# Performance work log

Hardware: AMD Instinct MI355X
Metric: run time of the kernel (lower is better)

Reference implementation:

```python
import jax, jax.numpy as jnp
import numpy as np

D_MODEL = 1024
D_STATE = 16
D_CONV = 4
EXPAND = 2
D_INNER = EXPAND * D_MODEL          # 2048
DT_RANK = (D_MODEL + 15) // 16      # 64 (mamba 'auto')
B, L = 2, 1024


def _mamba_params(key, scale=0.02):
    ks = jax.random.split(key, 6)
    return dict(
        inW=jax.random.normal(ks[0], (2 * D_INNER, D_MODEL), jnp.float32) * scale,
        convW=jax.random.normal(ks[1], (D_INNER, 1, D_CONV), jnp.float32) * scale,
        convb=jnp.zeros((D_INNER,), jnp.float32),
        xprojW=jax.random.normal(ks[2], (DT_RANK + 2 * D_STATE, D_INNER), jnp.float32) * scale,
        dtW=jax.random.normal(ks[3], (D_INNER, DT_RANK), jnp.float32) * scale,
        dtb=jax.random.normal(ks[4], (D_INNER,), jnp.float32) * scale,
        A_log=jnp.log(jnp.tile(jnp.arange(1, D_STATE + 1, dtype=jnp.float32), (D_INNER, 1))),
        Dskip=jnp.ones((D_INNER,), jnp.float32),
        outW=jax.random.normal(ks[5], (D_MODEL, D_INNER), jnp.float32) * scale,
    )


def setup_inputs() -> dict:
    key = jax.random.key(0)
    kx, kf, kb, kp = jax.random.split(key, 4)
    inp = {"x": jax.random.normal(kx, (B, L, D_MODEL), jnp.float32)}
    inp["ln_w"] = jnp.ones((D_MODEL,), jnp.float32)
    inp["ln_b"] = jnp.zeros((D_MODEL,), jnp.float32)
    for pref, k in (("f_", kf), ("b_", kb)):
        for name, v in _mamba_params(k).items():
            inp[pref + name] = v
    inp["proj_W"] = jax.random.normal(kp, (D_MODEL, 2 * D_MODEL), jnp.float32) * 0.02
    inp["proj_b"] = jnp.zeros((D_MODEL,), jnp.float32)
    return inp


def _layernorm(x, w, b, eps=1e-5):
    mu = jnp.mean(x, axis=-1, keepdims=True)
    var = jnp.var(x, axis=-1, keepdims=True)
    return (x - mu) * jax.lax.rsqrt(var + eps) * w + b


def _mamba(x, inW, convW, convb, xprojW, dtW, dtb, A_log, Dskip, outW):
    # x: [B, L, d_model]
    xz = jnp.einsum('bld,ed->ble', x, inW)           # [B,L,2*d_inner]
    xs, z = jnp.split(xz, 2, axis=-1)                # each [B,L,d_inner]
    # depthwise causal conv over L
    xc = jnp.transpose(xs, (0, 2, 1))                # [B,d_inner,L]
    xc = jax.lax.conv_general_dilated(
        xc, convW, window_strides=(1,), padding=[(D_CONV - 1, 0)],
        feature_group_count=D_INNER)
    xs = jax.nn.silu(jnp.transpose(xc + convb[None, :, None], (0, 2, 1)))
    # input-dependent dt, B, C
    xdb = jnp.einsum('bld,ed->ble', xs, xprojW)      # [B,L,dt_rank+2*d_state]
    dt, Bm, Cm = jnp.split(xdb, [DT_RANK, DT_RANK + D_STATE], axis=-1)
    dt = jax.nn.softplus(jnp.einsum('blr,dr->bld', dt, dtW) + dtb)  # [B,L,d_inner]
    A = -jnp.exp(A_log)                              # [d_inner,d_state], negative
    dA = jnp.exp(dt[..., None] * A)                  # [B,L,d_inner,d_state]
    dBx = dt[..., None] * Bm[:, :, None, :] * xs[..., None]

    def step(h, inputs):
        dA_t, dBx_t, C_t = inputs                    # [B,d,s],[B,d,s],[B,s]
        h = h * dA_t + dBx_t
        y = jnp.einsum('bds,bs->bd', h, C_t)
        return h, y

    h0 = jnp.zeros((x.shape[0], D_INNER, D_STATE), x.dtype)
    _, ys = jax.lax.scan(step, h0, (jnp.moveaxis(dA, 1, 0),
                                    jnp.moveaxis(dBx, 1, 0),
                                    jnp.moveaxis(Cm, 1, 0)))
    y = jnp.moveaxis(ys, 0, 1)                       # [B,L,d_inner]
    y = (y + xs * Dskip) * jax.nn.silu(z)
    return jnp.einsum('bld,ed->ble', y, outW)        # [B,L,d_model]


def reference(x, ln_w, ln_b,
              f_inW, f_convW, f_convb, f_xprojW, f_dtW, f_dtb, f_A_log, f_Dskip, f_outW,
              b_inW, b_convW, b_convb, b_xprojW, b_dtW, b_dtb, b_A_log, b_Dskip, b_outW,
              proj_W, proj_b):
    normed = _layernorm(x, ln_w, ln_b)
    fwd_out = _mamba(normed, f_inW, f_convW, f_convb, f_xprojW, f_dtW, f_dtb,
                     f_A_log, f_Dskip, f_outW)
    bwd_out = _mamba(normed[:, ::-1, :], b_inW, b_convW, b_convb, b_xprojW, b_dtW,
                     b_dtb, b_A_log, b_Dskip, b_outW)[:, ::-1, :]
    combined = jnp.concatenate([fwd_out, bwd_out], axis=-1)
    return x + jnp.einsum('blc,ec->ble', combined, proj_W) + proj_b
```

## Files before the change

### kernel.cpp

```cpp
#include <hip/hip_runtime.h>
#include <hip/hip_bf16.h>
#include <math.h>

#define DM   1024
#define DI   2048
#define DTR  64
#define DST  16
#define NB   2
#define LL   1024
#define MR   (NB*LL)
#define XLD  128
#define KS   8

typedef __bf16 bf16x8 __attribute__((ext_vector_type(8)));
typedef float  f32x4  __attribute__((ext_vector_type(4)));
typedef unsigned short u16x8 __attribute__((ext_vector_type(8)));

__device__ __forceinline__ float siluf(float x) { return x / (1.f + __expf(-x)); }
__device__ __forceinline__ float softplusf(float x) {
    return fmaxf(x, 0.f) + log1pf(__expf(-fabsf(x)));
}
__device__ __forceinline__ unsigned short f2bf(float f) {
    __hip_bfloat16 h = __float2bfloat16(f);
    return *reinterpret_cast<unsigned short*>(&h);
}
__device__ __forceinline__ float bf2f(__hip_bfloat16 h) { return __bfloat162float(h); }
__device__ __forceinline__ float bfu2f(unsigned short u) {
    __hip_bfloat16 h = *reinterpret_cast<__hip_bfloat16*>(&u);
    return __bfloat162float(h);
}

__device__ __forceinline__ void gl2lds16(const __hip_bfloat16* g, __hip_bfloat16* l)
{
    __builtin_amdgcn_global_load_lds(
        (const __attribute__((address_space(1))) unsigned int*)g,
        (__attribute__((address_space(3))) unsigned int*)l, 16, 0, 0);
}

__global__ __launch_bounds__(256) void prep_k(
    const float* __restrict__ s0, const float* __restrict__ s1,
    const float* __restrict__ s2, const float* __restrict__ s3,
    const float* __restrict__ s4, __hip_bfloat16* __restrict__ warena,
    const float* __restrict__ fx, const float* __restrict__ bx,
    __hip_bfloat16* __restrict__ wpb2,
    const float* __restrict__ fo, const float* __restrict__ bo,
    __hip_bfloat16* __restrict__ wot,
    const float* __restrict__ x, const float* __restrict__ lnw,
    const float* __restrict__ lnb, __hip_bfloat16* __restrict__ nb)
{
    __shared__ float pshm[64 * 65];
    const int b = blockIdx.x;
    const int tid = threadIdx.x;

    if (b < 10496) {
        long idx = (long)b * 1024 + tid * 4;
        const float* src; long off;
        if      (idx <  4194304L) { src = s0; off = idx; }
        else if (idx <  8388608L) { src = s1; off = idx -  4194304L; }
        else if (idx < 10485760L) { src = s2; off = idx -  8388608L; }
        else if (idx < 10616832L) { src = s3; off = idx - 10485760L; }
        else                      { src = s4; off = idx - 10616832L; }
        float4 v = *(const float4*)(src + off);
        ushort4 o;
        o.x = f2bf(v.x); o.y = f2bf(v.y); o.z = f2bf(v.z); o.w = f2bf(v.w);
        *(ushort4*)((unsigned short*)warena + idx) = o;
    } else if (b < 10624) {
        int t = b - 10496;
        int z = t >> 6;
        const float* in = z ? bx : fx;
        int idx = ((t & 63) * 256 + tid) * 4;
        int row = idx >> 11;
        ushort4 o = make_ushort4(0, 0, 0, 0);
        if (row < 96) {
            float4 v = *(const float4*)(in + idx);
            o.x = f2bf(v.x); o.y = f2bf(v.y); o.z = f2bf(v.z); o.w = f2bf(v.w);
        }
        *(ushort4*)((unsigned short*)wpb2 + (size_t)z * 128 * DI + idx) = o;
    } else if (b < 11648) {
        int t = b - 10624;
        int z = t >> 9; t &= 511;
        const float* src = z ? bo : fo;
        int c0 = (t & 31) * 64;
        int r0 = (t >> 5) * 64;
        int tc = tid & 63;
        int tr = tid >> 6;
        #pragma unroll
        for (int ii = 0; ii < 16; ++ii) {
            int rl = tr + ii * 4;
            pshm[tc * 65 + rl] = src[(size_t)(r0 + rl) * DI + c0 + tc];
        }
        __syncthreads();
        __hip_bfloat16* dst = wot + (size_t)z * DI * DM;
        #pragma unroll
        for (int ii = 0; ii < 16; ++ii) {
            int cl = tr + ii * 4;
            dst[(size_t)(c0 + cl) * DM + r0 + tc] = __float2bfloat16(pshm[cl * 65 + tc]);
        }
    } else {
        int row = b - 11648;
        const float* xr = x + (size_t)row * DM;
        float4 v = *(const float4*)(xr + tid * 4);
        float s = v.x + v.y + v.z + v.w;
        float q = v.x*v.x + v.y*v.y + v.z*v.z + v.w*v.w;
        #pragma unroll
        for (int off = 32; off > 0; off >>= 1) {
            s += __shfl_xor(s, off, 64);
            q += __shfl_xor(q, off, 64);
        }
        int wv = tid >> 6;
        if ((tid & 63) == 0) { pshm[wv] = s; pshm[8 + wv] = q; }
        __syncthreads();
        s = pshm[0] + pshm[1] + pshm[2] + pshm[3];
        q = pshm[8] + pshm[9] + pshm[10] + pshm[11];
        float mu  = s * (1.f / DM);
        float var = q * (1.f / DM) - mu * mu;
        float rstd = rsqrtf(var + 1e-5f);
        float4 wv4 = *(const float4*)(lnw + tid * 4);
        float4 bv4 = *(const float4*)(lnb + tid * 4);
        ushort4 o;
        o.x = f2bf((v.x - mu) * rstd * wv4.x + bv4.x);
        o.y = f2bf((v.y - mu) * rstd * wv4.y + bv4.y);
        o.z = f2bf((v.z - mu) * rstd * wv4.z + bv4.z);
        o.w = f2bf((v.w - mu) * rstd * wv4.w + bv4.w);
        *(ushort4*)((unsigned short*)nb + (size_t)row * DM + tid * 4) = o;
    }
}

__global__ __launch_bounds__(512) void inproj256_k(
    const __hip_bfloat16* __restrict__ A,
    const __hip_bfloat16* __restrict__ Bmat,
    __hip_bfloat16* __restrict__ C)
{
    __shared__ __hip_bfloat16 smem[65536];
    const int tid = threadIdx.x;
    int id = blockIdx.x;
    int s  = (id & 7) * 32 + (id >> 3);
    const int z  = s >> 7;
    const int r  = s & 127;
    const int bm = (r & 7) * 256;
    const int bn = (r >> 3) * 256;
    const __hip_bfloat16* Az = A;
    const __hip_bfloat16* Bz = Bmat + (size_t)z * 2 * DI * DM;
    __hip_bfloat16* Cz = C + (size_t)z * MR * 2 * DI;

    const int wv   = tid >> 6;
    const int lane = tid & 63;
    const int wm   = wv >> 2;
    const int wn   = wv & 3;
    const int fr   = lane & 15;
    const int quad = lane >> 4;

    const int srow = tid >> 2;
    const int scol = 8 * ((tid & 3) ^ ((tid >> 3) & 3));
    const int kph  = (quad ^ ((fr >> 1) & 3)) * 8;

    __hip_bfloat16* const Asl = smem;
    __hip_bfloat16* const Bsl = smem + 32768;

    f32x4 acc[8][4] = {};
    bf16x8 aF[4], bB[4];

#define STG_A(TAU, KK) { \
    const int ub_ = (((TAU) & 1) * 2 + (KK)) * 8192; \
    const int gc_ = (TAU) * 64 + (KK) * 32 + scol; \
    gl2lds16(Az + (size_t)(bm + srow) * DM + gc_,       Asl + ub_ + tid * 8); \
    gl2lds16(Az + (size_t)(bm + 128 + srow) * DM + gc_, Asl + ub_ + 4096 + tid * 8); }
#define STG_B(TAU, KK) { \
    const int ub_ = (((TAU) & 1) * 2 + (KK)) * 8192; \
    const int gc_ = (TAU) * 64 + (KK) * 32 + scol; \
    gl2lds16(Bz + (size_t)(bn + srow) * DM + gc_,       Bsl + ub_ + tid * 8); \
    gl2lds16(Bz + (size_t)(bn + 128 + srow) * DM + gc_, Bsl + ub_ + 4096 + tid * 8); }

#define RD_A(BUF, KK, MH) { \
    const __hip_bfloat16* p_ = Asl + ((BUF) * 2 + (KK)) * 8192 + kph; \
    _Pragma("unroll") for (int i = 0; i < 4; ++i) \
        aF[i] = *(const bf16x8*)(p_ + (wm * 128 + (MH) * 64 + i * 16 + fr) * 32); }
#define RD_B(BUF, KK) { \
    const __hip_bfloat16* p_ = Bsl + ((BUF) * 2 + (KK)) * 8192 + kph; \
    _Pragma("unroll") for (int j = 0; j < 4; ++j) \
        bB[j] = *(const bf16x8*)(p_ + (wn * 64 + j * 16 + fr) * 32); }

#define PHASE(BUF, KK, MH, STGC, T1, T2, VMC) { \
    if ((MH) == 0) { RD_B(BUF, KK); } \
    RD_A(BUF, KK, MH); \
    if ((STGC) == 1) { STG_A((T1), 1); } \
    if ((STGC) == 2) { STG_B((T1), 1); } \
    if ((STGC) == 3) { STG_A((T2), 0); } \
    if ((STGC) == 4) { STG_B((T2), 0); } \
    asm volatile("s_barrier" ::: "memory"); \
    asm volatile("s_waitcnt lgkmcnt(0)" ::: "memory"); \
    __builtin_amdgcn_sched_barrier(0); \
    __builtin_amdgcn_s_setprio(1); \
    _Pragma("unroll") for (int i = 0; i < 4; ++i) \
        _Pragma("unroll") for (int j = 0; j < 4; ++j) \
            acc[(MH) * 4 + i][j] = __builtin_amdgcn_mfma_f32_16x16x32_bf16( \
                aF[i], bB[j], acc[(MH) * 4 + i][j], 0, 0, 0); \
    __builtin_amdgcn_s_setprio(0); \
    if ((VMC) == 8) { asm volatile("s_waitcnt vmcnt(8)" ::: "memory"); } \
    if ((VMC) == 4) { asm volatile("s_waitcnt vmcnt(4)" ::: "memory"); } \
    if ((VMC) == 1) { asm volatile("s_waitcnt vmcnt(0)" ::: "memory"); } \
    asm volatile("s_barrier" ::: "memory"); }

    STG_A(0, 0); STG_B(0, 0); STG_A(0, 1); STG_B(0, 1); STG_A(1, 0); STG_B(1, 0);
    asm volatile("s_waitcnt vmcnt(8)" ::: "memory");
    asm volatile("s_barrier" ::: "memory");

    #pragma unroll 1
    for (int t = 0; t < 14; ++t) {
        const int buf = t & 1;
        const int t1 = t + 1, t2 = t + 2;
        PHASE(buf, 0, 0, 1, t1, t2, 0);
        PHASE(buf, 0, 1, 2, t1, t2, 8);
        PHASE(buf, 1, 0, 3, t1, t2, 0);
        PHASE(buf, 1, 1, 4, t1, t2, 8);
    }
    PHASE(0, 0, 0, 1, 15, 0, 0);
    PHASE(0, 0, 1, 2, 15, 0, 8);
    PHASE(0, 1, 0, 0, 0, 0, 0);
    PHASE(0, 1, 1, 0, 0, 0, 4);
    PHASE(1, 0, 0, 0, 0, 0, 0);
    PHASE(1, 0, 1, 0, 0, 0, 1);
    PHASE(1, 1, 0, 0, 0, 0, 0);
    PHASE(1, 1, 1, 0, 0, 0, 0);

#undef PHASE
#undef RD_A
#undef RD_B
#undef STG_A
#undef STG_B

    float* eps = (float*)smem;
    const int orow = tid >> 3;
    const int ocol = (tid & 7) * 32;
    #pragma unroll
    for (int p = 0; p < 4; ++p) {
        __syncthreads();
        if (wm == (p >> 1)) {
            int ib = (p & 1) * 4;
            #pragma unroll
            for (int i2 = 0; i2 < 4; ++i2)
                #pragma unroll
                for (int j = 0; j < 4; ++j)
                    #pragma unroll
                    for (int rr = 0; rr < 4; ++rr)
                        eps[(i2 * 16 + quad * 4 + rr) * 260 + wn * 64 + j * 16 + fr]
                            = acc[ib + i2][j][rr];
        }
        __syncthreads();
        unsigned short os[32] __attribute__((aligned(16)));
        #pragma unroll
        for (int c = 0; c < 32; ++c) os[c] = f2bf(eps[orow * 260 + ocol + c]);
        unsigned short* dst = (unsigned short*)Cz +
            (size_t)(bm + p * 64 + orow) * (2 * DI) + bn + ocol;
        *(uint4*)(dst +  0) = *(const uint4*)(os +  0);
        *(uint4*)(dst +  8) = *(const uint4*)(os +  8);
        *(uint4*)(dst + 16) = *(const uint4*)(os + 16);
        *(uint4*)(dst + 24) = *(const uint4*)(os + 24);
    }
}

template<int EPI>
__global__ __launch_bounds__(256) void gemm_gl(
    const __hip_bfloat16* __restrict__ A, int lda, size_t aofs,
    const __hip_bfloat16* __restrict__ B, int ldb, size_t bofs,
    void* __restrict__ Cp, int ldc, size_t cofs, int K,
    const float* __restrict__ bias0, const float* __restrict__ bias1)
{
    __shared__ __hip_bfloat16 smem[2 * 128 * 64];
    __hip_bfloat16* As = smem;
    __hip_bfloat16* Bs = smem + 128 * 64;
    const int tid  = threadIdx.x;
    const int z    = blockIdx.z;
    const int bm   = blockIdx.y * 128;
    const int bn   = blockIdx.x * 128;
    const __hip_bfloat16* Az = A + (size_t)z * aofs;
    const __hip_bfloat16* Bz = B + (size_t)z * bofs;
    const int wv   = tid >> 6;
    const int lane = tid & 63;
    const int wr   = (wv >> 1) * 64;
    const int wc   = (wv & 1) * 64;
    const int srow = wv * 32 + (lane >> 3);
    const int cg   = ((lane & 7) ^ (lane >> 3)) * 8;
    const int fr   = lane & 15;
    const int quad = lane >> 4;
    const int pc0  = (quad ^ (fr & 7)) * 8;
    const int pc1  = ((4 + quad) ^ (fr & 7)) * 8;

    f32x4 acc[4][4] = {};

    for (int k0 = 0; k0 < K; k0 += 64) {
        __syncthreads();
        #pragma unroll
        for (int i = 0; i < 4; ++i) {
            int r = srow + i * 8;
            gl2lds16(Az + (size_t)(bm + r) * lda + k0 + cg, As + wv * 2048 + i * 512);
            gl2lds16(Bz + (size_t)(bn + r) * ldb + k0 + cg, Bs + wv * 2048 + i * 512);
        }
        __syncthreads();
        #pragma unroll
        for (int kk = 0; kk < 2; ++kk) {
            const int pc = kk ? pc1 : pc0;
            bf16x8 af[4], bf_[4];
            #pragma unroll
            for (int i = 0; i < 4; ++i) {
                af[i]  = *(const bf16x8*)(As + (wr + i * 16 + fr) * 64 + pc);
                bf_[i] = *(const bf16x8*)(Bs + (wc + i * 16 + fr) * 64 + pc);
            }
            #pragma unroll
            for (int i = 0; i < 4; ++i)
                #pragma unroll
                for (int j = 0; j < 4; ++j)
                    acc[i][j] = __builtin_amdgcn_mfma_f32_16x16x32_bf16(
                        af[i], bf_[j], acc[i][j], 0, 0, 0);
        }
    }

    const float* bias = (EPI == 3) ? (z ? bias1 : bias0) : nullptr;
    float* eps = (float*)smem;
    const int half = wv >> 1;
    const int lrow = tid >> 3;
    const int cseg = (tid & 7) * 16;
    const int gr_  = bm + (lrow >> 4) * 64 + (lrow & 15);
    #pragma unroll
    for (int i = 0; i < 4; ++i) {
        __syncthreads();
        #pragma unroll
        for (int j = 0; j < 4; ++j)
            #pragma unroll
            for (int r = 0; r < 4; ++r)
                eps[(half * 16 + quad * 4 + r) * 132 + wc + j * 16 + fr] = acc[i][j][r];
        __syncthreads();
        float vals[16];
        *(float4*)(vals +  0) = *(const float4*)(eps + lrow * 132 + cseg +  0);
        *(float4*)(vals +  4) = *(const float4*)(eps + lrow * 132 + cseg +  4);
        *(float4*)(vals +  8) = *(const float4*)(eps + lrow * 132 + cseg +  8);
        *(float4*)(vals + 12) = *(const float4*)(eps + lrow * 132 + cseg + 12);
        int gr = gr_ + i * 16;
        int gc = bn + cseg;
        if (EPI == 0) {
            float* dst = (float*)Cp + (size_t)z * cofs + (size_t)gr * ldc + gc;
            *(float4*)(dst +  0) = *(const float4*)(vals +  0);
            *(float4*)(dst +  4) = *(const float4*)(vals +  4);
            *(float4*)(dst +  8) = *(const float4*)(vals +  8);
            *(float4*)(dst + 12) = *(const float4*)(vals + 12);
        } else {
            unsigned short os[16];
            #pragma unroll
            for (int c = 0; c < 16; ++c) {
                float t = vals[c];
                if (EPI == 3) t = softplusf(t + bias[gc + c]);
                os[c] = f2bf(t);
            }
            unsigned short* dst = (unsigned short*)Cp + (size_t)z * cofs +
                                  (size_t)gr * ldc + gc;
            *(ushort4*)(dst +  0) = *(ushort4*)(os +  0);
            *(ushort4*)(dst +  4) = *(ushort4*)(os +  4);
            *(ushort4*)(dst +  8) = *(ushort4*)(os +  8);
            *(ushort4*)(dst + 12) = *(ushort4*)(os + 12);
        }
    }
}

__global__ __launch_bounds__(256) void xproj_part_k(
    const __hip_bfloat16* __restrict__ A,
    const __hip_bfloat16* __restrict__ B,
    float* __restrict__ part)
{
    __shared__ __hip_bfloat16 smem[2 * 128 * 64];
    __hip_bfloat16* As = smem;
    __hip_bfloat16* Bs = smem + 128 * 64;
    const int tid  = threadIdx.x;
    const int ks   = blockIdx.x;
    const int bm   = blockIdx.y * 128;
    const int z    = blockIdx.z;
    const __hip_bfloat16* Az = A + (size_t)z * MR * DI;
    const __hip_bfloat16* Bz = B + (size_t)z * 128 * DI;
    const int kb   = ks * (DI / KS);
    const int wv   = tid >> 6;
    const int lane = tid & 63;
    const int wr   = (wv >> 1) * 64;
    const int wc   = (wv & 1) * 64;
    const int srow = wv * 32 + (lane >> 3);
    const int cg   = ((lane & 7) ^ (lane >> 3)) * 8;
    const int fr   = lane & 15;
    const int quad = lane >> 4;
    const int pc0  = (quad ^ (fr & 7)) * 8;
    const int pc1  = ((4 + quad) ^ (fr & 7)) * 8;

    f32x4 acc[4][4] = {};

    #pragma unroll
    for (int k0 = 0; k0 < DI / KS; k0 += 64) {
        __syncthreads();
        #pragma unroll
        for (int i = 0; i < 4; ++i) {
            int r = srow + i * 8;
            gl2lds16(Az + (size_t)(bm + r) * DI + kb + k0 + cg, As + wv * 2048 + i * 512);
            gl2lds16(Bz + (size_t)r * DI + kb + k0 + cg,        Bs + wv * 2048 + i * 512);
        }
        __syncthreads();
        #pragma unroll
        for (int kk = 0; kk < 2; ++kk) {
            const int pc = kk ? pc1 : pc0;
            bf16x8 af[4], bf_[4];
            #pragma unroll
            for (int i = 0; i < 4; ++i) {
                af[i]  = *(const bf16x8*)(As + (wr + i * 16 + fr) * 64 + pc);
                bf_[i] = *(const bf16x8*)(Bs + (wc + i * 16 + fr) * 64 + pc);
            }
            #pragma unroll
            for (int i = 0; i < 4; ++i)
                #pragma unroll
                for (int j = 0; j < 4; ++j)
                    acc[i][j] = __builtin_amdgcn_mfma_f32_16x16x32_bf16(
                        af[i], bf_[j], acc[i][j], 0, 0, 0);
        }
    }

    float* dst = part + ((size_t)z * KS + ks) * MR * XLD;
    const int er = quad * 4;
    #pragma unroll
    for (int i = 0; i < 4; ++i)
        #pragma unroll
        for (int j = 0; j < 4; ++j) {
            int row = bm + wr + i * 16 + er;
            int col = wc + j * 16 + fr;
            #pragma unroll
            for (int r = 0; r < 4; ++r)
                dst[(size_t)(row + r) * XLD + col] = acc[i][j][r];
        }
}

__global__ __launch_bounds__(256) void xproj_reduce_k(
    const float* __restrict__ part, float* __restrict__ xdb,
    __hip_bfloat16* __restrict__ xdbt)
{
    int z = blockIdx.y;
    size_t idx = ((size_t)blockIdx.x * 256 + threadIdx.x) * 4;
    const float* p = part + (size_t)z * KS * MR * XLD;
    float4 s = make_float4(0.f, 0.f, 0.f, 0.f);
    #pragma unroll
    for (int ks = 0; ks < KS; ++ks) {
        float4 v = *(const float4*)(p + (size_t)ks * MR * XLD + idx);
        s.x += v.x; s.y += v.y; s.z += v.z; s.w += v.w;
    }
    *(float4*)(xdb + (size_t)z * MR * XLD + idx) = s;
    int c = (int)(idx & (XLD - 1));
    if (c < 64) {
        size_t m = idx >> 7;
        ushort4 o;
        o.x = f2bf(s.x); o.y = f2bf(s.y); o.z = f2bf(s.z); o.w = f2bf(s.w);
        *(ushort4*)((unsigned short*)xdbt + (size_t)z * MR * 64 + m * 64 + c) = o;
    }
}

__global__ __launch_bounds__(256) void conv_silu_k(
    const __hip_bfloat16* __restrict__ xz2,
    const float* __restrict__ fW, const float* __restrict__ fb,
    const float* __restrict__ bW, const float* __restrict__ bb_,
    __hip_bfloat16* __restrict__ xsb2)
{
    const int dirv  = blockIdx.y;
    const int chunk = blockIdx.x;
    const int bb    = chunk >> 8;
    const int t0    = (chunk & 255) * 4;
    const int d     = threadIdx.x * 8;

    const float* w    = (dirv ? bW : fW) + d * 4;
    const float* bias = (dirv ? bb_ : fb) + d;
    const unsigned short* xz =
        (const unsigned short*)(xz2 + (size_t)dirv * MR * 2 * DI) + d;

    u16x8 rows[7];
    #pragma unroll
    for (int rr = 0; rr < 7; ++rr) {
        int t = dirv ? (t0 + rr) : (t0 - 3 + rr);
        bool ok = dirv ? (t < LL) : (t >= 0);
        u16x8 v = {};
        if (ok) v = *(const u16x8*)(xz + (size_t)(bb * LL + t) * (2 * DI));
        rows[rr] = v;
    }
    float wq[8][4];
    #pragma unroll
    for (int c = 0; c < 8; ++c) {
        float4 t = *(const float4*)(w + c * 4);
        if (dirv) { wq[c][0] = t.w; wq[c][1] = t.z; wq[c][2] = t.y; wq[c][3] = t.x; }
        else      { wq[c][0] = t.x; wq[c][1] = t.y; wq[c][2] = t.z; wq[c][3] = t.w; }
    }
    float4 b0 = *(const float4*)(bias);
    float4 b1 = *(const float4*)(bias + 4);
    float bs[8] = {b0.x, b0.y, b0.z, b0.w, b1.x, b1.y, b1.z, b1.w};

    unsigned short* outp = (unsigned short*)xsb2 + (size_t)dirv * MR * DI +
                           (size_t)(bb * LL + t0) * DI + d;
    #pragma unroll
    for (int o = 0; o < 4; ++o) {
        unsigned short os[8] __attribute__((aligned(16)));
        #pragma unroll
        for (int c = 0; c < 8; ++c) {
            float a = bs[c];
            #pragma unroll
            for (int k = 0; k < 4; ++k)
                a = fmaf(wq[c][k], bfu2f(rows[o + k][c]), a);
            os[c] = f2bf(siluf(a));
        }
        *(uint4*)(outp + (size_t)o * DI) = *(const uint4*)os;
    }
}

__global__ __launch_bounds__(256) void scan1_k(
    const __hip_bfloat16* __restrict__ dtf2, const __hip_bfloat16* __restrict__ xsb2,
    const float* __restrict__ xdb2,
    const float* __restrict__ fA, const float* __restrict__ bA,
    float* __restrict__ hend, float* __restrict__ aprod, int G, int Cn)
{
    int d  = blockIdx.x * 256 + threadIdx.x;
    int bb = blockIdx.y;
    int zz = blockIdx.z;
    int dirv = (zz >= G) ? 1 : 0;
    int g = zz - (dirv ? G : 0);
    const float* A_log = dirv ? bA : fA;
    const __hip_bfloat16* dtf = dtf2 + (size_t)dirv * MR * DI;
    const __hip_bfloat16* xs = xsb2 + (size_t)dirv * MR * DI;
    const float* xdb = xdb2 + (size_t)dirv * MR * XLD;
    size_t hoff = (size_t)dirv * G * (NB * DI * DST);

    float Ad[DST], h[DST], ap[DST];
    bool pw = true;
    #pragma unroll
    for (int s = 0; s < DST; ++s) {
        Ad[s] = -__expf(A_log[d * DST + s]);
        pw = pw && (fabsf(Ad[s] + (float)(s + 1)) < 1e-3f * (s + 1));
        h[s] = 0.f; ap[s] = 1.f;
    }
    int i0 = g * Cn;
    for (int i = 0; i < Cn; ++i) {
        int ii = i0 + i;
        int t = dirv ? (LL - 1 - ii) : ii;
        size_t m = (size_t)bb * LL + t;
        float dtv = bf2f(dtf[m * DI + d]);
        float xv  = bf2f(xs[m * DI + d]);
        const float* bc = xdb + m * XLD;
        float dtx = dtv * xv;
        float dAv[DST];
        if (pw) {
            float r = __expf(-dtv);
            float a = r;
            #pragma unroll
            for (int s = 0; s < DST; ++s) { dAv[s] = a; a *= r; }
        } else {
            #pragma unroll
            for (int s = 0; s < DST; ++s) dAv[s] = __expf(dtv * Ad[s]);
        }
        #pragma unroll
        for (int s = 0; s < DST; ++s) {
            h[s] = fmaf(h[s], dAv[s], dtx * bc[64 + s]);
            ap[s] *= dAv[s];
        }
    }
    size_t base = hoff + ((size_t)(g * NB + bb) * DI + d) * DST;
    #pragma unroll
    for (int s = 0; s < DST; s += 4) {
        *(float4*)(hend  + base + s) = make_float4(h[s], h[s+1], h[s+2], h[s+3]);
        *(float4*)(aprod + base + s) = make_float4(ap[s], ap[s+1], ap[s+2], ap[s+3]);
    }
}

__global__ __launch_bounds__(256) void scan2_k(
    float* __restrict__ hend, const float* __restrict__ aprod, int G)
{
    int dirv = blockIdx.y;
    int idx = blockIdx.x * 256 + threadIdx.x;
    const int slab = NB * DI * DST;
    size_t hoff = (size_t)dirv * G * slab;
    float carry = 0.f;
    for (int g = 0; g < G; ++g) {
        size_t off = hoff + (size_t)g * slab + idx;
        float a = aprod[off];
        float e = hend[off];
        hend[off] = carry;
        carry = fmaf(a, carry, e);
    }
}

__global__ __launch_bounds__(256) void scan3_k(
    const __hip_bfloat16* __restrict__ dtf2, const __hip_bfloat16* __restrict__ xsb2,
    const float* __restrict__ xdb2, const __hip_bfloat16* __restrict__ xz2,
    const float* __restrict__ fA, const float* __restrict__ bA,
    const float* __restrict__ fD, const float* __restrict__ bD,
    const float* __restrict__ hin, __hip_bfloat16* __restrict__ ycat, int G, int Cn)
{
    int d  = blockIdx.x * 256 + threadIdx.x;
    int bb = blockIdx.y;
    int zz = blockIdx.z;
    int dirv = (zz >= G) ? 1 : 0;
    int g = zz - (dirv ? G : 0);
    const float* A_log = dirv ? bA : fA;
    const float* Dskip = dirv ? bD : fD;
    const __hip_bfloat16* dtf = dtf2 + (size_t)dirv * MR * DI;
    const __hip_bfloat16* xs = xsb2 + (size_t)dirv * MR * DI;
    const float* xdb = xdb2 + (size_t)dirv * MR * XLD;
    const __hip_bfloat16* xz = xz2 + (size_t)dirv * MR * 2 * DI;
    size_t hoff = (size_t)dirv * G * (NB * DI * DST);

    float Ad[DST], h[DST];
    bool pw = true;
    size_t base = hoff + ((size_t)(g * NB + bb) * DI + d) * DST;
    #pragma unroll
    for (int s = 0; s < DST; ++s) {
        Ad[s] = -__expf(A_log[d * DST + s]);
        pw = pw && (fabsf(Ad[s] + (float)(s + 1)) < 1e-3f * (s + 1));
        h[s] = hin[base + s];
    }
    float Dsk = Dskip[d];
    int i0 = g * Cn;
    for (int i = 0; i < Cn; ++i) {
        int ii = i0 + i;
        int t = dirv ? (LL - 1 - ii) : ii;
        size_t m = (size_t)bb * LL + t;
        float dtv = bf2f(dtf[m * DI + d]);
        float xv  = bf2f(xs[m * DI + d]);
        const float* bc = xdb + m * XLD;
        float dtx = dtv * xv;
        float dAv[DST];
        if (pw) {
            float r = __expf(-dtv);
            float a = r;
            #pragma unroll
            for (int s = 0; s < DST; ++s) { dAv[s] = a; a *= r; }
        } else {
            #pragma unroll
            for (int s = 0; s < DST; ++s) dAv[s] = __expf(dtv * Ad[s]);
        }
        float yv = 0.f;
        #pragma unroll
        for (int s = 0; s < DST; ++s) {
            h[s] = fmaf(h[s], dAv[s], dtx * bc[64 + s]);
            yv = fmaf(h[s], bc[80 + s], yv);
        }
        float zv = bf2f(xz[m * (2 * DI) + DI + d]);
        ycat[m * (2 * DI) + (size_t)dirv * DI + d] =
            __float2bfloat16((yv + xv * Dsk) * siluf(zv));
    }
}

__global__ __launch_bounds__(256) void scan_mono_k(
    const __hip_bfloat16* __restrict__ dtf2, const __hip_bfloat16* __restrict__ xsb2,
    const float* __restrict__ xdb2, const __hip_bfloat16* __restrict__ xz2,
    const float* __restrict__ fA, const float* __restrict__ bA,
    const float* __restrict__ fD, const float* __restrict__ bD,
    __hip_bfloat16* __restrict__ ycat)
{
    int d  = blockIdx.x * 256 + threadIdx.x;
    int bb = blockIdx.y;
    int dirv = blockIdx.z;
    const float* A_log = dirv ? bA : fA;
    const float* Dskip = dirv ? bD : fD;
    const __hip_bfloat16* dtf = dtf2 + (size_t)dirv * MR * DI;
    const __hip_bfloat16* xs = xsb2 + (size_t)dirv * MR * DI;
    const float* xdb = xdb2 + (size_t)dirv * MR * XLD;
    const __hip_bfloat16* xz = xz2 + (size_t)dirv * MR * 2 * DI;
    float Ad[DST], h[DST];
    #pragma unroll
    for (int s = 0; s < DST; ++s) { Ad[s] = -__expf(A_log[d * DST + s]); h[s] = 0.f; }
    float Dsk = Dskip[d];
    for (int i = 0; i < LL; ++i) {
        int t = dirv ? (LL - 1 - i) : i;
        size_t m = (size_t)bb * LL + t;
        float dtv = bf2f(dtf[m * DI + d]);
        float xv  = bf2f(xs[m * DI + d]);
        const float* bc = xdb + m * XLD;
        float dtx = dtv * xv;
        float yv = 0.f;
        #pragma unroll
        for (int s = 0; s < DST; ++s) {
            float dA = __expf(dtv * Ad[s]);
            h[s] = fmaf(h[s], dA, dtx * bc[64 + s]);
            yv = fmaf(h[s], bc[80 + s], yv);
        }
        float zv = bf2f(xz[m * (2 * DI) + DI + d]);
        ycat[m * (2 * DI) + (size_t)dirv * DI + d] =
            __float2bfloat16((yv + xv * Dsk) * siluf(zv));
    }
}

__global__ __launch_bounds__(256) void final_reduce_k(
    const float* __restrict__ part, const float* __restrict__ x,
    const float* __restrict__ proj_b, float* __restrict__ out)
{
    size_t idx = ((size_t)blockIdx.x * 256 + threadIdx.x) * 4;
    float4 s = make_float4(0.f, 0.f, 0.f, 0.f);
    #pragma unroll
    for (int z = 0; z < 4; ++z) {
        float4 v = *(const float4*)(part + (size_t)z * MR * DM + idx);
        s.x += v.x; s.y += v.y; s.z += v.z; s.w += v.w;
    }
    float4 xv = *(const float4*)(x + idx);
    float4 pb = *(const float4*)(proj_b + (idx & (DM - 1)));
    float4 o;
    o.x = xv.x + pb.x + s.x;
    o.y = xv.y + pb.y + s.y;
    o.z = xv.z + pb.z + s.z;
    o.w = xv.w + pb.w + s.w;
    *(float4*)(out + idx) = o;
}

extern "C" void kernel_launch(void* const* d_in, const int* in_sizes, int n_in,
                              void* d_out, int out_size, void* d_ws, size_t ws_size,
                              hipStream_t stream)
{
    const float* x      = (const float*)d_in[0];
    const float* ln_w   = (const float*)d_in[1];
    const float* ln_b   = (const float*)d_in[2];
    const float* f_inW    = (const float*)d_in[3];
    const float* f_convW  = (const float*)d_in[4];
    const float* f_convb  = (const float*)d_in[5];
    const float* f_xprojW = (const float*)d_in[6];
    const float* f_dtW    = (const float*)d_in[7];
    const float* f_dtb    = (const float*)d_in[8];
    const float* f_A_log  = (const float*)d_in[9];
    const float* f_Dskip  = (const float*)d_in[10];
    const float* f_outW   = (const float*)d_in[11];
    const float* b_inW    = (const float*)d_in[12];
    const float* b_convW  = (const float*)d_in[13];
    const float* b_convb  = (const float*)d_in[14];
    const float* b_xprojW = (const float*)d_in[15];
    const float* b_dtW    = (const float*)d_in[16];
    const float* b_dtb    = (const float*)d_in[17];
    const float* b_A_log  = (const float*)d_in[18];
    const float* b_Dskip  = (const float*)d_in[19];
    const float* b_outW   = (const float*)d_in[20];
    const float* proj_W = (const float*)d_in[21];
    const float* proj_b = (const float*)d_in[22];

    float* ws = (float*)d_ws;
    size_t o = 0;
    __hip_bfloat16* xz2  = (__hip_bfloat16*)(ws + o);
    float* fpart = ws + o;
    o += (size_t)2 * MR * 2 * DI / 2;
    __hip_bfloat16* xsb2 = (__hip_bfloat16*)(ws + o); o += (size_t)2 * MR * DI / 2;
    __hip_bfloat16* ycat = (__hip_bfloat16*)(ws + o);
    float* xpart = ws + o;
    o += (size_t)MR * 2 * DI / 2;
    float* xdb2 = ws + o; o += (size_t)2 * MR * XLD;
    __hip_bfloat16* xdbt = (__hip_bfloat16*)(ws + o); o += (size_t)2 * MR * 64 / 2;
    __hip_bfloat16* dtfb = (__hip_bfloat16*)(ws + o); o += (size_t)2 * MR * DI / 2;
    __hip_bfloat16* nb = (__hip_bfloat16*)(ws + o); o += (size_t)MR * DM / 2;
    __hip_bfloat16* warena = (__hip_bfloat16*)(ws + o); o += 15466496 / 2;
    float* hbuf = ws + o;
    size_t base_floats = o;

    __hip_bfloat16* wbi  = warena;
    __hip_bfloat16* pwb  = warena +  8388608;
    __hip_bfloat16* wdt  = warena + 10485760;
    __hip_bfloat16* wpb2 = warena + 10747904;
    __hip_bfloat16* wcat = warena + 11272192;

    const size_t slab = (size_t)NB * DI * DST;
    int G = 32;
    while (G > 4 && (base_floats + 4ull * G * slab) * 4 > ws_size) G >>= 1;
    int useChunks = ((base_floats + 4ull * G * slab) * 4 <= ws_size);
    float* hend  = hbuf;
    float* aprod = hbuf + 2ull * G * slab;
    int Cn = useChunks ? LL / G : LL;

    int wotInHbuf = useChunks && (4ull * G * slab >= 2097152ull);
    __hip_bfloat16* wot = wotInHbuf ? (__hip_bfloat16*)hbuf : xz2;

    prep_k<<<13696, 256, 0, stream>>>(
        f_inW, b_inW, proj_W, f_dtW, b_dtW, warena,
        f_xprojW, b_xprojW, wpb2,
        f_outW, b_outW, wot,
        x, ln_w, ln_b, nb);

    if (wotInHbuf) {
        inproj256_k<<<256, 512, 0, stream>>>(nb, wbi, xz2);
        gemm_gl<1><<<dim3(DI / 128, DM / 128, 2), 256, 0, stream>>>(
            pwb, 2 * DM, (size_t)DM, wot, DM, (size_t)DI * DM,
            wcat, 2 * DI, (size_t)DI, DM, nullptr, nullptr);
    } else {
        gemm_gl<1><<<dim3(DI / 128, DM / 128, 2), 256, 0, stream>>>(
            pwb, 2 * DM, (size_t)DM, wot, DM, (size_t)DI * DM,
            wcat, 2 * DI, (size_t)DI, DM, nullptr, nullptr);
        inproj256_k<<<256, 512, 0, stream>>>(nb, wbi, xz2);
    }

    conv_silu_k<<<dim3(MR / 4, 2), 256, 0, stream>>>(
        xz2, f_convW, f_convb, b_convW, b_convb, xsb2);

    xproj_part_k<<<dim3(KS, MR / 128, 2), 256, 0, stream>>>(xsb2, wpb2, xpart);
    xproj_reduce_k<<<dim3((MR * XLD) / 1024, 2), 256, 0, stream>>>(xpart, xdb2, xdbt);

    gemm_gl<3><<<dim3(DI / 128, MR / 128, 2), 256, 0, stream>>>(
        xdbt, 64, (size_t)MR * 64, wdt, 64, (size_t)DI * 64,
        dtfb, DI, (size_t)MR * DI, 64, f_dtb, b_dtb);

    if (useChunks) {
        scan1_k<<<dim3(DI / 256, NB, 2 * G), 256, 0, stream>>>(
            dtfb, xsb2, xdb2, f_A_log, b_A_log, hend, aprod, G, Cn);
        scan2_k<<<dim3((NB * DI * DST) / 256, 2), 256, 0, stream>>>(hend, aprod, G);
        scan3_k<<<dim3(DI / 256, NB, 2 * G), 256, 0, stream>>>(
            dtfb, xsb2, xdb2, xz2, f_A_log, b_A_log, f_Dskip, b_Dskip,
            hend, ycat, G, Cn);
    } else {
        scan_mono_k<<<dim3(DI / 256, NB, 2), 256, 0, stream>>>(
            dtfb, xsb2, xdb2, xz2, f_A_log, b_A_log, f_Dskip, b_Dskip, ycat);
    }

    gemm_gl<0><<<dim3(DM / 128, MR / 128, 4), 256, 0, stream>>>(
        ycat, 2 * DI, 1024, wcat, 2 * DI, 1024,
        fpart, DM, (size_t)MR * DM, 1024, nullptr, nullptr);

    final_reduce_k<<<(MR * DM) / 1024, 256, 0, stream>>>(
        fpart, x, proj_b, (float*)d_out);
}
```

Baseline: 396.3 us.

## Replace split-K output GEMM and reduce with fused 64x64 outproj kernel

The final projection was a split-K GEMM with four fp32 partial slabs followed by a separate reduction kernel that added x and the bias. It becomes a single 64x64-tile MFMA kernel that runs the full K=4096 loop and writes out = x + bias + acc directly. This removes the partial-buffer traffic and one launch, but the new kernel has no double-buffering and only 512 blocks. Separately, the weight-conversion part of prep_k now converts 4096 elements per block instead of 1024, so far fewer blocks are launched.

```diff
diff --git a/kernel.cpp b/kernel.cpp
--- a/kernel.cpp
+++ b/kernel.cpp
@@ -52,20 +52,24 @@
     const int b = blockIdx.x;
     const int tid = threadIdx.x;
 
-    if (b < 10496) {
-        long idx = (long)b * 1024 + tid * 4;
+    if (b < 2624) {
+        long base = (long)b * 4096;
         const float* src; long off;
-        if      (idx <  4194304L) { src = s0; off = idx; }
-        else if (idx <  8388608L) { src = s1; off = idx -  4194304L; }
-        else if (idx < 10485760L) { src = s2; off = idx -  8388608L; }
-        else if (idx < 10616832L) { src = s3; off = idx - 10485760L; }
-        else                      { src = s4; off = idx - 10616832L; }
-        float4 v = *(const float4*)(src + off);
-        ushort4 o;
-        o.x = f2bf(v.x); o.y = f2bf(v.y); o.z = f2bf(v.z); o.w = f2bf(v.w);
-        *(ushort4*)((unsigned short*)warena + idx) = o;
-    } else if (b < 10624) {
-        int t = b - 10496;
+        if      (base <  4194304L) { src = s0; off = base; }
+        else if (base <  8388608L) { src = s1; off = base -  4194304L; }
+        else if (base < 10485760L) { src = s2; off = base -  8388608L; }
+        else if (base < 10616832L) { src = s3; off = base - 10485760L; }
+        else                       { src = s4; off = base - 10616832L; }
+        #pragma unroll
+        for (int j = 0; j < 4; ++j) {
+            long e = (long)j * 1024 + tid * 4;
+            float4 v = *(const float4*)(src + off + e);
+            ushort4 o;
+            o.x = f2bf(v.x); o.y = f2bf(v.y); o.z = f2bf(v.z); o.w = f2bf(v.w);
+            *(ushort4*)((unsigned short*)warena + base + e) = o;
+        }
+    } else if (b < 2752) {
+        int t = b - 2624;
         int z = t >> 6;
         const float* in = z ? bx : fx;
         int idx = ((t & 63) * 256 + tid) * 4;
@@ -76,8 +80,8 @@
             o.x = f2bf(v.x); o.y = f2bf(v.y); o.z = f2bf(v.z); o.w = f2bf(v.w);
         }
         *(ushort4*)((unsigned short*)wpb2 + (size_t)z * 128 * DI + idx) = o;
-    } else if (b < 11648) {
-        int t = b - 10624;
+    } else if (b < 3776) {
+        int t = b - 2752;
         int z = t >> 9; t &= 511;
         const float* src = z ? bo : fo;
         int c0 = (t & 31) * 64;
@@ -97,7 +101,7 @@
             dst[(size_t)(c0 + cl) * DM + r0 + tc] = __float2bfloat16(pshm[cl * 65 + tc]);
         }
     } else {
-        int row = b - 11648;
+        int row = b - 3776;
         const float* xr = x + (size_t)row * DM;
         float4 v = *(const float4*)(xr + tid * 4);
         float s = v.x + v.y + v.z + v.w;
@@ -337,28 +341,89 @@
         *(float4*)(vals + 12) = *(const float4*)(eps + lrow * 132 + cseg + 12);
         int gr = gr_ + i * 16;
         int gc = bn + cseg;
-        if (EPI == 0) {
-            float* dst = (float*)Cp + (size_t)z * cofs + (size_t)gr * ldc + gc;
-            *(float4*)(dst +  0) = *(const float4*)(vals +  0);
-            *(float4*)(dst +  4) = *(const float4*)(vals +  4);
-            *(float4*)(dst +  8) = *(const float4*)(vals +  8);
-            *(float4*)(dst + 12) = *(const float4*)(vals + 12);
-        } else {
-            unsigned short os[16];
-            #pragma unroll
-            for (int c = 0; c < 16; ++c) {
-                float t = vals[c];
-                if (EPI == 3) t = softplusf(t + bias[gc + c]);
-                os[c] = f2bf(t);
+        unsigned short os[16];
+        #pragma unroll
+        for (int c = 0; c < 16; ++c) {
+            float t = vals[c];
+            if (EPI == 3) t = softplusf(t + bias[gc + c]);
+            os[c] = f2bf(t);
+        }
+        unsigned short* dst = (unsigned short*)Cp + (size_t)z * cofs +
+                              (size_t)gr * ldc + gc;
+        *(ushort4*)(dst +  0) = *(ushort4*)(os +  0);
+        *(ushort4*)(dst +  4) = *(ushort4*)(os +  4);
+        *(ushort4*)(dst +  8) = *(ushort4*)(os +  8);
+        *(ushort4*)(dst + 12) = *(ushort4*)(os + 12);
+    }
+}
+
+__global__ __launch_bounds__(256) void outproj_k(
+    const __hip_bfloat16* __restrict__ A,
+    const __hip_bfloat16* __restrict__ Bm,
+    const float* __restrict__ x, const float* __restrict__ proj_b,
+    float* __restrict__ out)
+{
+    __shared__ __hip_bfloat16 smem[2 * 64 * 64];
+    __hip_bfloat16* As = smem;
+    __hip_bfloat16* Bs = smem + 64 * 64;
+    const int tid  = threadIdx.x;
+    const int bn   = blockIdx.x * 64;
+    const int bm   = blockIdx.y * 64;
+    const int wv   = tid >> 6;
+    const int lane = tid & 63;
+    const int wr   = (wv >> 1) * 32;
+    const int wc   = (wv & 1) * 32;
+    const int srow = wv * 16 + (lane >> 3);
+    const int cg   = ((lane & 7) ^ (lane >> 3)) * 8;
+    const int fr   = lane & 15;
+    const int quad = lane >> 4;
+    const int pc0  = (quad ^ (fr & 7)) * 8;
+    const int pc1  = ((4 + quad) ^ (fr & 7)) * 8;
+    const int K    = 2 * DI;
+
+    f32x4 acc[2][2] = {};
+
+    for (int k0 = 0; k0 < K; k0 += 64) {
+        __syncthreads();
+        #pragma unroll
+        for (int j = 0; j < 2; ++j) {
+            int r = srow + j * 8;
+            gl2lds16(A  + (size_t)(bm + r) * K + k0 + cg, As + wv * 1024 + j * 512);
+            gl2lds16(Bm + (size_t)(bn + r) * K + k0 + cg, Bs + wv * 1024 + j * 512);
+        }
+        __syncthreads();
+        #pragma unroll
+        for (int kk = 0; kk < 2; ++kk) {
+            const int pc = kk ? pc1 : pc0;
+            bf16x8 af[2], bf_[2];
+            #pragma unroll
+            for (int i = 0; i < 2; ++i) {
+                af[i]  = *(const bf16x8*)(As + (wr + i * 16 + fr) * 64 + pc);
+                bf_[i] = *(const bf16x8*)(Bs + (wc + i * 16 + fr) * 64 + pc);
             }
-            unsigned short* dst = (unsigned short*)Cp + (size_t)z * cofs +
-                                  (size_t)gr * ldc + gc;
-            *(ushort4*)(dst +  0) = *(ushort4*)(os +  0);
-            *(ushort4*)(dst +  4) = *(ushort4*)(os +  4);
-            *(ushort4*)(dst +  8) = *(ushort4*)(os +  8);
-            *(ushort4*)(dst + 12) = *(ushort4*)(os + 12);
-        }
-    }
+            #pragma unroll
+            for (int i = 0; i < 2; ++i)
+                #pragma unroll
+                for (int j = 0; j < 2; ++j)
+                    acc[i][j] = __builtin_amdgcn_mfma_f32_16x16x32_bf16(
+                        af[i], bf_[j], acc[i][j], 0, 0, 0);
+        }
+    }
+
+    const float pb0 = proj_b[bn + wc + fr];
+    const float pb1 = proj_b[bn + wc + 16 + fr];
+    #pragma unroll
+    for (int i = 0; i < 2; ++i)
+        #pragma unroll
+        for (int j = 0; j < 2; ++j) {
+            const int gc = bn + wc + j * 16 + fr;
+            const float pb = j ? pb1 : pb0;
+            #pragma unroll
+            for (int r = 0; r < 4; ++r) {
+                size_t off = (size_t)(bm + wr + i * 16 + quad * 4 + r) * DM + gc;
+                out[off] = x[off] + pb + acc[i][j][r];
+            }
+        }
 }
 
 __global__ __launch_bounds__(256) void xproj_part_k(
@@ -682,27 +747,6 @@
         ycat[m * (2 * DI) + (size_t)dirv * DI + d] =
             __float2bfloat16((yv + xv * Dsk) * siluf(zv));
     }
-}
-
-__global__ __launch_bounds__(256) void final_reduce_k(
-    const float* __restrict__ part, const float* __restrict__ x,
-    const float* __restrict__ proj_b, float* __restrict__ out)
-{
-    size_t idx = ((size_t)blockIdx.x * 256 + threadIdx.x) * 4;
-    float4 s = make_float4(0.f, 0.f, 0.f, 0.f);
-    #pragma unroll
-    for (int z = 0; z < 4; ++z) {
-        float4 v = *(const float4*)(part + (size_t)z * MR * DM + idx);
-        s.x += v.x; s.y += v.y; s.z += v.z; s.w += v.w;
-    }
-    float4 xv = *(const float4*)(x + idx);
-    float4 pb = *(const float4*)(proj_b + (idx & (DM - 1)));
-    float4 o;
-    o.x = xv.x + pb.x + s.x;
-    o.y = xv.y + pb.y + s.y;
-    o.z = xv.z + pb.z + s.z;
-    o.w = xv.w + pb.w + s.w;
-    *(float4*)(out + idx) = o;
 }
 
 extern "C" void kernel_launch(void* const* d_in, const int* in_sizes, int n_in,
@@ -736,7 +780,6 @@
     float* ws = (float*)d_ws;
     size_t o = 0;
     __hip_bfloat16* xz2  = (__hip_bfloat16*)(ws + o);
-    float* fpart = ws + o;
     o += (size_t)2 * MR * 2 * DI / 2;
     __hip_bfloat16* xsb2 = (__hip_bfloat16*)(ws + o); o += (size_t)2 * MR * DI / 2;
     __hip_bfloat16* ycat = (__hip_bfloat16*)(ws + o);
@@ -767,7 +810,7 @@
     int wotInHbuf = useChunks && (4ull * G * slab >= 2097152ull);
     __hip_bfloat16* wot = wotInHbuf ? (__hip_bfloat16*)hbuf : xz2;
 
-    prep_k<<<13696, 256, 0, stream>>>(
+    prep_k<<<5824, 256, 0, stream>>>(
         f_inW, b_inW, proj_W, f_dtW, b_dtW, warena,
         f_xprojW, b_xprojW, wpb2,
         f_outW, b_outW, wot,
@@ -807,10 +850,6 @@
             dtfb, xsb2, xdb2, xz2, f_A_log, b_A_log, f_Dskip, b_Dskip, ycat);
     }
 
-    gemm_gl<0><<<dim3(DM / 128, MR / 128, 4), 256, 0, stream>>>(
-        ycat, 2 * DI, 1024, wcat, 2 * DI, 1024,
-        fpart, DM, (size_t)MR * DM, 1024, nullptr, nullptr);
-
-    final_reduce_k<<<(MR * DM) / 1024, 256, 0, stream>>>(
-        fpart, x, proj_b, (float*)d_out);
-}
+    outproj_k<<<dim3(DM / 64, MR / 64), 256, 0, stream>>>(
+        ycat, wcat, x, proj_b, (float*)d_out);
+}
```

After: 391.2 us. Within noise of the previous version (-1.3%).
